# Kernel optimization log

Measured on AMD Instinct MI355X. Metric: run time of the kernel, lower is better.

The kernel has to match this reference:

```python
import jax, jax.numpy as jnp
import numpy as np

N = 100000   # nodes
E = 1250000  # directed edges
F = 32       # node_features
H = 64       # hidden_channels
C = 10       # num_classes
NEG_SLOPE = 0.2  # GATConv default LeakyReLU slope


def _glorot(key, shape):
    fan_in = shape[0]
    return jax.random.normal(key, shape, jnp.float32) / np.sqrt(fan_in)


def setup_inputs() -> dict:
    k = jax.random.split(jax.random.key(0), 16)
    x = jax.random.normal(k[0], (N, F), jnp.float32)
    edge_index = jax.random.randint(k[1], (2, E), 0, N, dtype=jnp.int32)
    return {
        "x": x,
        "edge_index": edge_index,
        # GCNConv 1
        "W1": _glorot(k[2], (F, H)), "b1": jnp.zeros((H,), jnp.float32),
        # GATConv (heads=1)
        "W2": _glorot(k[3], (H, H)),
        "a_src": _glorot(k[4], (H,)), "a_dst": _glorot(k[5], (H,)),
        "b2": jnp.zeros((H,), jnp.float32),
        # GCNConv 3
        "W3": _glorot(k[6], (H, H)), "b3": jnp.zeros((H,), jnp.float32),
        # optimization head
        "Wopt": _glorot(k[7], (H, C)), "bopt": jnp.zeros((C,), jnp.float32),
        # bottleneck detector MLP
        "Wb1": _glorot(k[8], (H, 32)), "bb1": jnp.zeros((32,), jnp.float32),
        "Wb2": _glorot(k[9], (32, 1)), "bb2": jnp.zeros((1,), jnp.float32),
    }


def _gcn_conv(x, W, b, src, dst, n):
    # PyG GCNConv: self-loops already appended to src/dst by caller.
    h = x @ W  # [n, out]
    deg = jnp.zeros((n,), x.dtype).at[dst].add(1.0)
    dinv = jax.lax.rsqrt(jnp.maximum(deg, 1e-12))
    norm = dinv[src] * dinv[dst]  # [e]
    msg = h[src] * norm[:, None]  # gather + scale
    out = jnp.zeros_like(h).at[dst].add(msg)  # scatter-add
    return out + b


def _gat_conv(x, W, a_src, a_dst, b, src, dst, n):
    # PyG GATConv, heads=1: self-loops already appended.
    h = x @ W  # [n, out]
    alpha_s = h @ a_src  # [n]
    alpha_d = h @ a_dst  # [n]
    e = jax.nn.leaky_relu(alpha_s[src] + alpha_d[dst], NEG_SLOPE)  # [e]
    # softmax over incoming edges of each dst node
    emax = jax.ops.segment_max(e, dst, num_segments=n)
    p = jnp.exp(e - emax[dst])
    denom = jax.ops.segment_sum(p, dst, num_segments=n)
    alpha = p / denom[dst]
    out = jnp.zeros_like(h).at[dst].add(h[src] * alpha[:, None])
    return out + b


def reference(x, edge_index, W1, b1, W2, a_src, a_dst, b2, W3, b3,
              Wopt, bopt, Wb1, bb1, Wb2, bb2):
    n = x.shape[0]
    loops = jnp.arange(n, dtype=edge_index.dtype)
    src = jnp.concatenate([edge_index[0], loops])
    dst = jnp.concatenate([edge_index[1], loops])

    h = jax.nn.relu(_gcn_conv(x, W1, b1, src, dst, n))
    h = jax.nn.relu(_gat_conv(h, W2, a_src, a_dst, b2, src, dst, n))
    h = jax.nn.relu(_gcn_conv(h, W3, b3, src, dst, n))

    optimizations = h @ Wopt + bopt                     # [n, C]
    bottlenecks = jax.nn.sigmoid(jax.nn.relu(h @ Wb1 + bb1) @ Wb2 + bb2)  # [n, 1]
    graph_embedding = h.mean(axis=0)                    # [H]
    return optimizations, bottlenecks, graph_embedding
```

## Files before the change

### kernel.cpp

```cpp
#include <hip/hip_runtime.h>
#include <hip/hip_bf16.h>


#define CAP 64
#define NP2 128
#define NB2MAX 800

__device__ __forceinline__ int uwave(){
  return __builtin_amdgcn_readfirstlane(threadIdx.x >> 6);
}
__device__ __forceinline__ unsigned short f2bf(float f){
  unsigned u = __float_as_uint(f);
  return (unsigned short)((u + 0x7fffu + ((u >> 16) & 1u)) >> 16);
}
__device__ __forceinline__ float bfl(unsigned u){ return __uint_as_float(u << 16); }
__device__ __forceinline__ float bfh(unsigned u){ return __uint_as_float(u & 0xffff0000u); }
__device__ __forceinline__ float bfu(unsigned short s){ return __uint_as_float(((unsigned)s) << 16); }
__device__ __forceinline__ float rdlane(float v, int l){
  return __uint_as_float(__builtin_amdgcn_readlane(__float_as_uint(v), l));
}

__global__ void k_setup(const float* __restrict__ Wopt, const float* __restrict__ bopt,
                        const float* __restrict__ Wb1, const float* __restrict__ bb1,
                        float* __restrict__ Wcat, float* __restrict__ bcat,
                        int* __restrict__ bcnt, unsigned short* __restrict__ tb,
                        unsigned short* __restrict__ xh, float* __restrict__ emb_acc,
                        int n, int nb2){
  int i = blockIdx.x*blockDim.x + threadIdx.x;
  if (i < nb2) bcnt[i] = 0;
  if (blockIdx.x == 0){
    int tid = threadIdx.x;
    for (int j = tid; j < 4096; j += 256){
      int f = j >> 6, c = j & 63;
      float w = 0.f;
      if (c < 10)       w = Wopt[f*10 + c];
      else if (c >= 32) w = Wb1[f*32 + (c-32)];
      Wcat[j] = w;
    }
    if (tid < 64){
      float b = 0.f;
      if (tid < 10)       b = bopt[tid];
      else if (tid >= 32) b = bb1[tid-32];
      bcat[tid] = b;
      tb[(size_t)n*64 + tid] = 0;
      emb_acc[tid] = 0.f;
    }
    if (tid >= 64 && tid < 96) xh[(size_t)n*32 + (tid-64)] = 0;
  }
}

__global__ __launch_bounds__(256) void k_part(const int* __restrict__ src,
                        const int* __restrict__ dst,
                        uint2* __restrict__ pairs, int* __restrict__ bcnt,
                        int e, int nb2, int pbcap){
  __shared__ int lcnt[NB2MAX];
  __shared__ int lbase[NB2MAX];
  int tid = threadIdx.x;
  for (int j = tid; j < nb2; j += 256) lcnt[j] = 0;
  __syncthreads();
  int i0 = blockIdx.x*2048 + tid*8;
  int d[8], s[8], bk[8], lp[8];
  int nv = e - i0;
  if (nv > 8) nv = 8;
  if (nv < 0) nv = 0;
  if (nv == 8){
    int4 d0 = *(const int4*)(dst + i0), d1 = *(const int4*)(dst + i0 + 4);
    int4 s0 = *(const int4*)(src + i0), s1 = *(const int4*)(src + i0 + 4);
    d[0]=d0.x; d[1]=d0.y; d[2]=d0.z; d[3]=d0.w;
    d[4]=d1.x; d[5]=d1.y; d[6]=d1.z; d[7]=d1.w;
    s[0]=s0.x; s[1]=s0.y; s[2]=s0.z; s[3]=s0.w;
    s[4]=s1.x; s[5]=s1.y; s[6]=s1.z; s[7]=s1.w;
  } else {
    #pragma unroll
    for (int j = 0; j < 8; j++){ d[j] = 0; s[j] = 0; }
    for (int j = 0; j < nv; j++){ d[j] = dst[i0+j]; s[j] = src[i0+j]; }
  }
  #pragma unroll
  for (int j = 0; j < 8; j++){
    if (j < nv){
      bk[j] = d[j] >> 7;
      lp[j] = atomicAdd(&lcnt[bk[j]], 1);
    }
  }
  __syncthreads();
  for (int j = tid; j < nb2; j += 256){
    int c = lcnt[j];
    if (c) lbase[j] = atomicAdd(&bcnt[j], c);
  }
  __syncthreads();
  #pragma unroll
  for (int j = 0; j < 8; j++){
    if (j < nv){
      int p = lbase[bk[j]] + lp[j];
      if (p < pbcap)
        pairs[(size_t)bk[j]*pbcap + p] = make_uint2((unsigned)d[j], (unsigned)s[j]);
    }
  }
}

__global__ __launch_bounds__(256) void k_fill(const uint2* __restrict__ pairs,
                        const int* __restrict__ bcnt, int* __restrict__ cnt,
                        int* __restrict__ adj, int pbcap, int n){
  __shared__ int lc[NP2];
  __shared__ int ladj[NP2*CAP];
  int b = blockIdx.x;
  int lo = b << 7;
  int nn = min(NP2, n - lo);
  int tid = threadIdx.x;
  for (int j = tid; j < NP2; j += 256) lc[j] = 0;
  __syncthreads();
  int m = bcnt[b];
  if (m > pbcap) m = pbcap;
  const uint2* pb = pairs + (size_t)b*pbcap;
  for (int j = tid; j < m; j += 256){
    uint2 p = pb[j];
    int r = (int)p.x - lo;
    int pos = atomicAdd(&lc[r], 1);
    if (pos < CAP) ladj[(r << 6) + pos] = (int)p.y;
  }
  __syncthreads();
  if (tid < nn) cnt[lo + tid] = lc[tid];
  int tot = nn << 4;
  uint4* ga = (uint4*)(adj + (size_t)lo*CAP);
  const uint4* la = (const uint4*)ladj;
  for (int j = tid; j < tot; j += 256) ga[j] = la[j];
}

__global__ void k_castscale(const float* __restrict__ x, const int* __restrict__ cnt,
                            unsigned short* __restrict__ xh, int total4){
  int i = blockIdx.x*blockDim.x + threadIdx.x;
  if (i >= total4) return;
  int row = i >> 3;
  float dv = rsqrtf((float)(cnt[row] + 1));
  float4 v = ((const float4*)x)[i];
  uint2 o;
  o.x = (unsigned)f2bf(v.x*dv) | ((unsigned)f2bf(v.y*dv) << 16);
  o.y = (unsigned)f2bf(v.z*dv) | ((unsigned)f2bf(v.w*dv) << 16);
  ((uint2*)xh)[i] = o;
}

__global__ __launch_bounds__(256) void k_agg32g(const unsigned short* __restrict__ xh,
                          const int* __restrict__ adj, const int* __restrict__ cnt,
                          const float* __restrict__ W1, const float* __restrict__ b1,
                          unsigned short* __restrict__ h, int n){
  int lane = threadIdx.x & 63;
  float wreg[32];
  #pragma unroll
  for (int k = 0; k < 32; k++) wreg[k] = W1[k*64 + lane];
  float br = b1[lane];
  int v0 = blockIdx.x*8 + uwave()*2;
  if (v0 >= n) return;
  int v1 = v0 + 1;
  bool has1 = v1 < n;
  if (!has1) v1 = v0;
  int cn0 = cnt[v0], cn1 = cnt[v1];
  int c0 = min(cn0, CAP), c1 = min(cn1, CAP);
  int ureg0 = n, ureg1 = n;
  if (lane < c0) ureg0 = (adj + (size_t)v0*CAP)[lane];
  if (lane < c1) ureg1 = (adj + (size_t)v1*CAP)[lane];
  int g = lane >> 3, q = lane & 7;
  float4 a0 = {0.f,0.f,0.f,0.f}, a1 = {0.f,0.f,0.f,0.f};
  int itm = (max(c0, c1) + 7) >> 3;
  #pragma unroll 2
  for (int jj = 0; jj < itm; jj++){
    int u0 = __shfl(ureg0, jj*8 + g);
    int u1 = __shfl(ureg1, jj*8 + g);
    uint2 r0 = ((const uint2*)(xh + (size_t)u0*32))[q];
    uint2 r1 = ((const uint2*)(xh + (size_t)u1*32))[q];
    a0.x += bfl(r0.x); a0.y += bfh(r0.x); a0.z += bfl(r0.y); a0.w += bfh(r0.y);
    a1.x += bfl(r1.x); a1.y += bfh(r1.x); a1.z += bfl(r1.y); a1.w += bfh(r1.y);
  }
  #pragma unroll
  for (int off = 8; off <= 32; off <<= 1){
    a0.x += __shfl_xor(a0.x, off); a0.y += __shfl_xor(a0.y, off);
    a0.z += __shfl_xor(a0.z, off); a0.w += __shfl_xor(a0.w, off);
    a1.x += __shfl_xor(a1.x, off); a1.y += __shfl_xor(a1.y, off);
    a1.z += __shfl_xor(a1.z, off); a1.w += __shfl_xor(a1.w, off);
  }
  uint2 s0 = ((const uint2*)(xh + (size_t)v0*32))[q];
  uint2 s1 = ((const uint2*)(xh + (size_t)v1*32))[q];
  a0.x += bfl(s0.x); a0.y += bfh(s0.x); a0.z += bfl(s0.y); a0.w += bfh(s0.y);
  a1.x += bfl(s1.x); a1.y += bfh(s1.x); a1.z += bfl(s1.y); a1.w += bfh(s1.y);
  float dv0 = rsqrtf((float)(cn0 + 1)), dv1 = rsqrtf((float)(cn1 + 1));
  a0.x *= dv0; a0.y *= dv0; a0.z *= dv0; a0.w *= dv0;
  a1.x *= dv1; a1.y *= dv1; a1.z *= dv1; a1.w *= dv1;
  float h0 = br, h1v = br;
  #pragma unroll
  for (int q2 = 0; q2 < 8; q2++){
    float w0x = rdlane(a0.x, q2), w1x = rdlane(a1.x, q2);
    float w0y = rdlane(a0.y, q2), w1y = rdlane(a1.y, q2);
    float w0z = rdlane(a0.z, q2), w1z = rdlane(a1.z, q2);
    float w0w = rdlane(a0.w, q2), w1w = rdlane(a1.w, q2);
    h0 = fmaf(w0x, wreg[q2*4+0], h0); h1v = fmaf(w1x, wreg[q2*4+0], h1v);
    h0 = fmaf(w0y, wreg[q2*4+1], h0); h1v = fmaf(w1y, wreg[q2*4+1], h1v);
    h0 = fmaf(w0z, wreg[q2*4+2], h0); h1v = fmaf(w1z, wreg[q2*4+2], h1v);
    h0 = fmaf(w0w, wreg[q2*4+3], h0); h1v = fmaf(w1w, wreg[q2*4+3], h1v);
  }
  h[(size_t)v0*64 + lane] = f2bf(fmaxf(h0, 0.f));
  if (has1) h[(size_t)v1*64 + lane] = f2bf(fmaxf(h1v, 0.f));
}

template<bool SCALE>
__global__ __launch_bounds__(256, 4) void k_gemm_b(const unsigned short* __restrict__ x,
                       const float* __restrict__ W, const int* __restrict__ cnt,
                       unsigned short* __restrict__ t, int n){
  int lane = threadIdx.x & 63;
  int gw = blockIdx.x*4 + uwave();
  int nw = gridDim.x*4;
  float wreg[64];
  #pragma unroll
  for (int k = 0; k < 64; k++) wreg[k] = W[k*64 + lane];
  for (int v = gw; v < n; v += nw){
    const uint4* xr = (const uint4*)(x + (size_t)v*64);
    float acc = 0.f;
    #pragma unroll
    for (int k8 = 0; k8 < 8; k8++){
      uint4 c = xr[k8];
      acc = fmaf(bfl(c.x), wreg[k8*8+0], acc);
      acc = fmaf(bfh(c.x), wreg[k8*8+1], acc);
      acc = fmaf(bfl(c.y), wreg[k8*8+2], acc);
      acc = fmaf(bfh(c.y), wreg[k8*8+3], acc);
      acc = fmaf(bfl(c.z), wreg[k8*8+4], acc);
      acc = fmaf(bfh(c.z), wreg[k8*8+5], acc);
      acc = fmaf(bfl(c.w), wreg[k8*8+6], acc);
      acc = fmaf(bfh(c.w), wreg[k8*8+7], acc);
    }
    if (SCALE) acc *= rsqrtf((float)(cnt[v] + 1));
    t[(size_t)v*64 + lane] = f2bf(acc);
  }
}

__global__ __launch_bounds__(256, 4) void k_gemm_alpha(const unsigned short* __restrict__ x,
                       const float* __restrict__ W,
                       const float* __restrict__ asrc, const float* __restrict__ adst,
                       unsigned short* __restrict__ t, float* __restrict__ als,
                       float* __restrict__ ald, int n){
  int lane = threadIdx.x & 63;
  int gw = blockIdx.x*4 + uwave();
  int nw = gridDim.x*4;
  float wreg[64];
  #pragma unroll
  for (int k = 0; k < 64; k++) wreg[k] = W[k*64 + lane];
  float asr = asrc[lane], adr = adst[lane];
  for (int v = gw; v < n; v += nw){
    const uint4* xr = (const uint4*)(x + (size_t)v*64);
    float acc = 0.f;
    #pragma unroll
    for (int k8 = 0; k8 < 8; k8++){
      uint4 c = xr[k8];
      acc = fmaf(bfl(c.x), wreg[k8*8+0], acc);
      acc = fmaf(bfh(c.x), wreg[k8*8+1], acc);
      acc = fmaf(bfl(c.y), wreg[k8*8+2], acc);
      acc = fmaf(bfh(c.y), wreg[k8*8+3], acc);
      acc = fmaf(bfl(c.z), wreg[k8*8+4], acc);
      acc = fmaf(bfh(c.z), wreg[k8*8+5], acc);
      acc = fmaf(bfl(c.w), wreg[k8*8+6], acc);
      acc = fmaf(bfh(c.w), wreg[k8*8+7], acc);
    }
    t[(size_t)v*64 + lane] = f2bf(acc);
    float s1 = acc * asr, s2 = acc * adr;
    #pragma unroll
    for (int off = 32; off; off >>= 1){
      s1 += __shfl_xor(s1, off);
      s2 += __shfl_xor(s2, off);
    }
    if (lane == 0){ als[v] = s1; ald[v] = s2; }
  }
}

__global__ __launch_bounds__(256) void k_gcn_agg(const unsigned short* __restrict__ t,
                          const int* __restrict__ adj, const int* __restrict__ cnt,
                          const float* __restrict__ b, unsigned short* __restrict__ h, int n){
  int lane = threadIdx.x & 63;
  int v = blockIdx.x*4 + uwave();
  if (v >= n) return;
  int cn = cnt[v];
  int c = min(cn, CAP);
  const int* row = adj + (size_t)v*CAP;
  float acc = bfu(t[(size_t)v*64 + lane]);
  int j = 0;
  for (; j + 3 < c; j += 4){
    int u0 = row[j], u1 = row[j+1], u2 = row[j+2], u3 = row[j+3];
    float x0 = bfu(t[(size_t)u0*64 + lane]);
    float x1 = bfu(t[(size_t)u1*64 + lane]);
    float x2 = bfu(t[(size_t)u2*64 + lane]);
    float x3 = bfu(t[(size_t)u3*64 + lane]);
    acc += x0; acc += x1; acc += x2; acc += x3;
  }
  for (; j < c; j++){
    int u0 = row[j];
    acc += bfu(t[(size_t)u0*64 + lane]);
  }
  float dv = rsqrtf((float)(cn + 1));
  float out = fmaxf(fmaf(acc, dv, b[lane]), 0.f);
  h[(size_t)v*64 + lane] = f2bf(out);
}

__global__ __launch_bounds__(256) void k_gat_agg(const unsigned short* __restrict__ t,
                          const int* __restrict__ adj, const int* __restrict__ cnt,
                          const float* __restrict__ als, const float* __restrict__ ald,
                          const float* __restrict__ b, unsigned short* __restrict__ h, int n){
  int lane = threadIdx.x & 63;
  int v = blockIdx.x*4 + uwave();
  if (v >= n) return;
  int c = min(cnt[v], CAP);
  const int* row = adj + (size_t)v*CAP;
  int ureg = v;
  if (lane < c) ureg = row[lane];
  float adv = ald[v];
  float e = als[ureg] + adv;
  e = e > 0.f ? e : 0.2f*e;
  float es = als[v] + adv; es = es > 0.f ? es : 0.2f*es;
  float em = (lane < c) ? e : -1e30f;
  #pragma unroll
  for (int off = 32; off; off >>= 1) em = fmaxf(em, __shfl_xor(em, off));
  em = fmaxf(em, es);
  float p = (lane < c) ? __expf(e - em) : 0.f;
  float sm = p;
  #pragma unroll
  for (int off = 32; off; off >>= 1) sm += __shfl_xor(sm, off);
  float ps = __expf(es - em);
  float inv = 1.f / (sm + ps);
  float acc = ps * bfu(t[(size_t)v*64 + lane]);
  int j = 0;
  for (; j + 3 < c; j += 4){
    int u0 = row[j], u1 = row[j+1], u2 = row[j+2], u3 = row[j+3];
    float a0 = als[u0], a1 = als[u1], a2 = als[u2], a3 = als[u3];
    float x0 = bfu(t[(size_t)u0*64 + lane]);
    float x1 = bfu(t[(size_t)u1*64 + lane]);
    float x2 = bfu(t[(size_t)u2*64 + lane]);
    float x3 = bfu(t[(size_t)u3*64 + lane]);
    float e0 = a0 + adv; e0 = e0 > 0.f ? e0 : 0.2f*e0;
    float e1 = a1 + adv; e1 = e1 > 0.f ? e1 : 0.2f*e1;
    float e2 = a2 + adv; e2 = e2 > 0.f ? e2 : 0.2f*e2;
    float e3 = a3 + adv; e3 = e3 > 0.f ? e3 : 0.2f*e3;
    acc = fmaf(__expf(e0 - em), x0, acc);
    acc = fmaf(__expf(e1 - em), x1, acc);
    acc = fmaf(__expf(e2 - em), x2, acc);
    acc = fmaf(__expf(e3 - em), x3, acc);
  }
  for (; j < c; j++){
    int u0 = row[j];
    float a0 = als[u0];
    float x0 = bfu(t[(size_t)u0*64 + lane]);
    float e0 = a0 + adv; e0 = e0 > 0.f ? e0 : 0.2f*e0;
    acc = fmaf(__expf(e0 - em), x0, acc);
  }
  float out = fmaxf(fmaf(acc, inv, b[lane]), 0.f);
  h[(size_t)v*64 + lane] = f2bf(out);
}

__global__ __launch_bounds__(256, 4) void k_heads(const unsigned short* __restrict__ h,
                        const float* __restrict__ Wcat, const float* __restrict__ bcat,
                        const float* __restrict__ Wb2, const float* __restrict__ bb2,
                        float* __restrict__ out_opt, float* __restrict__ out_bot, int n){
  int lane = threadIdx.x & 63;
  int gw = blockIdx.x*4 + uwave();
  int nw = gridDim.x*4;
  float wreg[64];
  #pragma unroll
  for (int k = 0; k < 64; k++) wreg[k] = Wcat[k*64 + lane];
  float bcr  = bcat[lane];
  float wb2r = (lane >= 32) ? Wb2[lane-32] : 0.f;
  float bb2r = bb2[0];
  for (int v = gw; v < n; v += nw){
    const uint4* xr = (const uint4*)(h + (size_t)v*64);
    float acc = bcr;
    #pragma unroll
    for (int k8 = 0; k8 < 8; k8++){
      uint4 c = xr[k8];
      acc = fmaf(bfl(c.x), wreg[k8*8+0], acc);
      acc = fmaf(bfh(c.x), wreg[k8*8+1], acc);
      acc = fmaf(bfl(c.y), wreg[k8*8+2], acc);
      acc = fmaf(bfh(c.y), wreg[k8*8+3], acc);
      acc = fmaf(bfl(c.z), wreg[k8*8+4], acc);
      acc = fmaf(bfh(c.z), wreg[k8*8+5], acc);
      acc = fmaf(bfl(c.w), wreg[k8*8+6], acc);
      acc = fmaf(bfh(c.w), wreg[k8*8+7], acc);
    }
    if (lane < 10) out_opt[(size_t)v*10 + lane] = acc;
    float contrib = fmaxf(acc, 0.f) * wb2r;
    #pragma unroll
    for (int off = 32; off; off >>= 1) contrib += __shfl_xor(contrib, off);
    if (lane == 0) out_bot[v] = 1.f / (1.f + __expf(-(contrib + bb2r)));
  }
}

__global__ __launch_bounds__(256) void k_mean(const unsigned short* __restrict__ h,
                       float* __restrict__ emb_acc, int n){
  __shared__ float red[256];
  int tid = threadIdx.x;
  int w = tid >> 6, lane = tid & 63;
  float s = 0.f;
  for (int r = blockIdx.x*4 + w; r < n; r += 1024)
    s += __uint_as_float(((unsigned)h[(size_t)r*64 + lane]) << 16);
  red[tid] = s;
  __syncthreads();
  if (tid < 64)
    atomicAdd(&emb_acc[tid], red[tid] + red[64+tid] + red[128+tid] + red[192+tid]);
}

__global__ void k_embed(const float* __restrict__ emb_acc, float* __restrict__ out_emb,
                        float invn){
  if (threadIdx.x < 64) out_emb[threadIdx.x] = emb_acc[threadIdx.x] * invn;
}

extern "C" void kernel_launch(void* const* d_in, const int* in_sizes, int n_in,
                              void* d_out, int out_size, void* d_ws, size_t ws_size,
                              hipStream_t stream) {
  const float* x    = (const float*)d_in[0];
  const int*   ei   = (const int*)d_in[1];
  const float* W1   = (const float*)d_in[2];
  const float* b1   = (const float*)d_in[3];
  const float* W2   = (const float*)d_in[4];
  const float* a_s  = (const float*)d_in[5];
  const float* a_d  = (const float*)d_in[6];
  const float* b2   = (const float*)d_in[7];
  const float* W3   = (const float*)d_in[8];
  const float* b3   = (const float*)d_in[9];
  const float* Wopt = (const float*)d_in[10];
  const float* bopt = (const float*)d_in[11];
  const float* Wb1  = (const float*)d_in[12];
  const float* bb1  = (const float*)d_in[13];
  const float* Wb2  = (const float*)d_in[14];
  const float* bb2  = (const float*)d_in[15];

  int n = in_sizes[0] / 32;
  int e = in_sizes[1] / 2;
  const int* src = ei;
  const int* dst = ei + e;

  char* ws = (char*)d_ws;
  size_t off = 0;
  auto alloc = [&](size_t bytes) -> void* {
    void* p = ws + off;
    off += (bytes + 255) & ~(size_t)255;
    return p;
  };
  int nb2 = (n + NP2 - 1) >> 7;
  int*            cnt     = (int*)           alloc((size_t)n * 4);
  int*            adj     = (int*)           alloc((size_t)n * CAP * 4);
  float*          als     = (float*)         alloc((size_t)n * 4);
  float*          ald     = (float*)         alloc((size_t)n * 4);
  unsigned short* xh      = (unsigned short*)alloc((size_t)(n+1) * 32 * 2);
  unsigned short* tb      = (unsigned short*)alloc((size_t)(n+1) * 64 * 2);
  unsigned short* hbuf    = (unsigned short*)alloc((size_t)n * 64 * 2);
  float*          emb_acc = (float*)         alloc((size_t)64 * 4);
  float*          Wcat    = (float*)         alloc((size_t)4096 * 4);
  float*          bcat    = (float*)         alloc((size_t)64 * 4);
  int*            bcnt    = (int*)           alloc((size_t)nb2 * 4);

  int pbcap = e / nb2 + 384;
  long pcap_max = ((long)n * 128) / ((long)nb2 * 8);
  if (pbcap > (int)pcap_max) pbcap = (int)pcap_max;
  uint2* pairs = (uint2*)hbuf;

  float* out_opt = (float*)d_out;
  float* out_bot = out_opt + (size_t)n * 10;
  float* out_emb = out_bot + n;

  int nb8    = (n + 7) / 8;
  int nb4    = (n + 3) / 4;
  int nbN    = (n + 255) / 256;
  int nbP    = (e + 2047) / 2048;
  int total4 = n*32/4;
  int nbC    = (total4 + 255) / 256;

  k_setup<<<nbN, 256, 0, stream>>>(Wopt, bopt, Wb1, bb1, Wcat, bcat,
                                   bcnt, tb, xh, emb_acc, n, nb2);
  k_part<<<nbP, 256, 0, stream>>>(src, dst, pairs, bcnt, e, nb2, pbcap);
  k_fill<<<nb2, 256, 0, stream>>>(pairs, bcnt, cnt, adj, pbcap, n);
  k_castscale<<<nbC, 256, 0, stream>>>(x, cnt, xh, total4);

  k_agg32g<<<nb8, 256, 0, stream>>>(xh, adj, cnt, W1, b1, hbuf, n);

  k_gemm_alpha<<<1024, 256, 0, stream>>>(hbuf, W2, a_s, a_d, tb, als, ald, n);
  k_gat_agg<<<nb4, 256, 0, stream>>>(tb, adj, cnt, als, ald, b2, hbuf, n);

  k_gemm_b<true><<<1024, 256, 0, stream>>>(hbuf, W3, cnt, tb, n);
  k_gcn_agg<<<nb4, 256, 0, stream>>>(tb, adj, cnt, b3, hbuf, n);

  k_heads<<<1024, 256, 0, stream>>>(hbuf, Wcat, bcat, Wb2, bb2,
                                    out_opt, out_bot, n);
  k_mean<<<256, 256, 0, stream>>>(hbuf, emb_acc, n);
  k_embed<<<1, 64, 0, stream>>>(emb_acc, out_emb, 1.0f / (float)n);
}
```

Before: 375.1 us.

## Process eight nodes per wavefront in GCN/GAT aggregation with 16-byte row gathers

The GCN and GAT aggregation kernels now assign 8 destination nodes per wavefront, with 8 lanes per node each loading a uint4 (8 bf16 features), instead of one node per wavefront with one feature per lane. Neighbor indices are loaded once per 8-slot block and broadcast with shuffles. The adjacency rows are pre-filled with a sentinel index n pointing at zeroed padding rows (tb and als), so lanes can run to the group-max degree without bounds checks. This is meant to cut the number of memory instructions and the per-edge index loads, at the cost of divergence padding up to the max degree among the 8 grouped nodes.

```diff
diff --git a/kernel.cpp b/kernel.cpp
--- a/kernel.cpp
+++ b/kernel.cpp
@@ -25,7 +25,7 @@
                         float* __restrict__ Wcat, float* __restrict__ bcat,
                         int* __restrict__ bcnt, unsigned short* __restrict__ tb,
                         unsigned short* __restrict__ xh, float* __restrict__ emb_acc,
-                        int n, int nb2){
+                        float* __restrict__ als, int n, int nb2){
   int i = blockIdx.x*blockDim.x + threadIdx.x;
   if (i < nb2) bcnt[i] = 0;
   if (blockIdx.x == 0){
@@ -44,6 +44,7 @@
       bcat[tid] = b;
       tb[(size_t)n*64 + tid] = 0;
       emb_acc[tid] = 0.f;
+      if (tid == 0) als[n] = 0.f;
     }
     if (tid >= 64 && tid < 96) xh[(size_t)n*32 + (tid-64)] = 0;
   }
@@ -108,6 +109,8 @@
   int nn = min(NP2, n - lo);
   int tid = threadIdx.x;
   for (int j = tid; j < NP2; j += 256) lc[j] = 0;
+  int4 nfill = make_int4(n, n, n, n);
+  for (int j = tid; j < NP2*CAP/4; j += 256) ((int4*)ladj)[j] = nfill;
   __syncthreads();
   int m = bcnt[b];
   if (m > pbcap) m = pbcap;
@@ -272,28 +275,48 @@
                           const int* __restrict__ adj, const int* __restrict__ cnt,
                           const float* __restrict__ b, unsigned short* __restrict__ h, int n){
   int lane = threadIdx.x & 63;
-  int v = blockIdx.x*4 + uwave();
-  if (v >= n) return;
-  int cn = cnt[v];
-  int c = min(cn, CAP);
-  const int* row = adj + (size_t)v*CAP;
-  float acc = bfu(t[(size_t)v*64 + lane]);
-  int j = 0;
-  for (; j + 3 < c; j += 4){
-    int u0 = row[j], u1 = row[j+1], u2 = row[j+2], u3 = row[j+3];
-    float x0 = bfu(t[(size_t)u0*64 + lane]);
-    float x1 = bfu(t[(size_t)u1*64 + lane]);
-    float x2 = bfu(t[(size_t)u2*64 + lane]);
-    float x3 = bfu(t[(size_t)u3*64 + lane]);
-    acc += x0; acc += x1; acc += x2; acc += x3;
-  }
-  for (; j < c; j++){
-    int u0 = row[j];
-    acc += bfu(t[(size_t)u0*64 + lane]);
-  }
+  int g = lane >> 3, q = lane & 7;
+  int v0 = blockIdx.x*32 + uwave()*8;
+  if (v0 >= n) return;
+  int vg = v0 + g;
+  bool vok = vg < n;
+  int vgc = vok ? vg : n - 1;
+  int cn = cnt[vgc];
+  int c = vok ? min(cn, CAP) : 0;
+  int cm = c;
+  cm = max(cm, __shfl_xor(cm, 8));
+  cm = max(cm, __shfl_xor(cm, 16));
+  cm = max(cm, __shfl_xor(cm, 32));
+  int cmax = __builtin_amdgcn_readfirstlane(cm);
+  const int* arow = adj + (size_t)vgc*CAP;
+  float a[8] = {0,0,0,0,0,0,0,0};
+  int bsel = (lane & 56);
+  for (int blk = 0; blk*8 < cmax; blk++){
+    int ureg = arow[blk*8 + q];
+    #pragma unroll
+    for (int j2 = 0; j2 < 8; j2++){
+      if (blk*8 + j2 >= cmax) break;
+      int u = __shfl(ureg, bsel | j2);
+      uint4 r = ((const uint4*)(t + (size_t)u*64))[q];
+      a[0] += bfl(r.x); a[1] += bfh(r.x); a[2] += bfl(r.y); a[3] += bfh(r.y);
+      a[4] += bfl(r.z); a[5] += bfh(r.z); a[6] += bfl(r.w); a[7] += bfh(r.w);
+    }
+  }
+  uint4 s = ((const uint4*)(t + (size_t)vgc*64))[q];
+  a[0] += bfl(s.x); a[1] += bfh(s.x); a[2] += bfl(s.y); a[3] += bfh(s.y);
+  a[4] += bfl(s.z); a[5] += bfh(s.z); a[6] += bfl(s.w); a[7] += bfh(s.w);
   float dv = rsqrtf((float)(cn + 1));
-  float out = fmaxf(fmaf(acc, dv, b[lane]), 0.f);
-  h[(size_t)v*64 + lane] = f2bf(out);
+  float4 b0 = ((const float4*)b)[2*q], b1v = ((const float4*)b)[2*q+1];
+  float r0 = fmaxf(fmaf(a[0], dv, b0.x), 0.f),  r1 = fmaxf(fmaf(a[1], dv, b0.y), 0.f);
+  float r2 = fmaxf(fmaf(a[2], dv, b0.z), 0.f),  r3 = fmaxf(fmaf(a[3], dv, b0.w), 0.f);
+  float r4 = fmaxf(fmaf(a[4], dv, b1v.x), 0.f), r5 = fmaxf(fmaf(a[5], dv, b1v.y), 0.f);
+  float r6 = fmaxf(fmaf(a[6], dv, b1v.z), 0.f), r7 = fmaxf(fmaf(a[7], dv, b1v.w), 0.f);
+  uint4 o;
+  o.x = (unsigned)f2bf(r0) | ((unsigned)f2bf(r1) << 16);
+  o.y = (unsigned)f2bf(r2) | ((unsigned)f2bf(r3) << 16);
+  o.z = (unsigned)f2bf(r4) | ((unsigned)f2bf(r5) << 16);
+  o.w = (unsigned)f2bf(r6) | ((unsigned)f2bf(r7) << 16);
+  if (vok) ((uint4*)(h + (size_t)vg*64))[q] = o;
 }
 
 __global__ __launch_bounds__(256) void k_gat_agg(const unsigned short* __restrict__ t,
@@ -301,53 +324,79 @@
                           const float* __restrict__ als, const float* __restrict__ ald,
                           const float* __restrict__ b, unsigned short* __restrict__ h, int n){
   int lane = threadIdx.x & 63;
-  int v = blockIdx.x*4 + uwave();
-  if (v >= n) return;
-  int c = min(cnt[v], CAP);
-  const int* row = adj + (size_t)v*CAP;
-  int ureg = v;
-  if (lane < c) ureg = row[lane];
-  float adv = ald[v];
-  float e = als[ureg] + adv;
-  e = e > 0.f ? e : 0.2f*e;
-  float es = als[v] + adv; es = es > 0.f ? es : 0.2f*es;
-  float em = (lane < c) ? e : -1e30f;
-  #pragma unroll
-  for (int off = 32; off; off >>= 1) em = fmaxf(em, __shfl_xor(em, off));
-  em = fmaxf(em, es);
-  float p = (lane < c) ? __expf(e - em) : 0.f;
-  float sm = p;
-  #pragma unroll
-  for (int off = 32; off; off >>= 1) sm += __shfl_xor(sm, off);
+  int g = lane >> 3, q = lane & 7;
+  int v0 = blockIdx.x*32 + uwave()*8;
+  if (v0 >= n) return;
+  int vg = v0 + g;
+  bool vok = vg < n;
+  int vgc = vok ? vg : n - 1;
+  int c = vok ? min(cnt[vgc], CAP) : 0;
+  int cm = c;
+  cm = max(cm, __shfl_xor(cm, 8));
+  cm = max(cm, __shfl_xor(cm, 16));
+  cm = max(cm, __shfl_xor(cm, 32));
+  int cmax = __builtin_amdgcn_readfirstlane(cm);
+  const int* arow = adj + (size_t)vgc*CAP;
+  float adv = ald[vgc];
+  float es = als[vgc] + adv; es = es > 0.f ? es : 0.2f*es;
+  float er[8];
+  float em = es;
+  #pragma unroll
+  for (int r = 0; r < 8; r++){
+    if (r*8 >= cmax) break;
+    int slot = r*8 + q;
+    int u = arow[slot];
+    float ev = als[u] + adv; ev = ev > 0.f ? ev : 0.2f*ev;
+    er[r] = (slot < c) ? ev : -1e30f;
+    em = fmaxf(em, er[r]);
+  }
+  em = fmaxf(em, __shfl_xor(em, 1));
+  em = fmaxf(em, __shfl_xor(em, 2));
+  em = fmaxf(em, __shfl_xor(em, 4));
+  float sm = 0.f;
+  #pragma unroll
+  for (int r = 0; r < 8; r++){
+    if (r*8 >= cmax) break;
+    sm += ((r*8 + q) < c) ? __expf(er[r] - em) : 0.f;
+  }
+  sm += __shfl_xor(sm, 1);
+  sm += __shfl_xor(sm, 2);
+  sm += __shfl_xor(sm, 4);
   float ps = __expf(es - em);
   float inv = 1.f / (sm + ps);
-  float acc = ps * bfu(t[(size_t)v*64 + lane]);
-  int j = 0;
-  for (; j + 3 < c; j += 4){
-    int u0 = row[j], u1 = row[j+1], u2 = row[j+2], u3 = row[j+3];
-    float a0 = als[u0], a1 = als[u1], a2 = als[u2], a3 = als[u3];
-    float x0 = bfu(t[(size_t)u0*64 + lane]);
-    float x1 = bfu(t[(size_t)u1*64 + lane]);
-    float x2 = bfu(t[(size_t)u2*64 + lane]);
-    float x3 = bfu(t[(size_t)u3*64 + lane]);
-    float e0 = a0 + adv; e0 = e0 > 0.f ? e0 : 0.2f*e0;
-    float e1 = a1 + adv; e1 = e1 > 0.f ? e1 : 0.2f*e1;
-    float e2 = a2 + adv; e2 = e2 > 0.f ? e2 : 0.2f*e2;
-    float e3 = a3 + adv; e3 = e3 > 0.f ? e3 : 0.2f*e3;
-    acc = fmaf(__expf(e0 - em), x0, acc);
-    acc = fmaf(__expf(e1 - em), x1, acc);
-    acc = fmaf(__expf(e2 - em), x2, acc);
-    acc = fmaf(__expf(e3 - em), x3, acc);
-  }
-  for (; j < c; j++){
-    int u0 = row[j];
-    float a0 = als[u0];
-    float x0 = bfu(t[(size_t)u0*64 + lane]);
-    float e0 = a0 + adv; e0 = e0 > 0.f ? e0 : 0.2f*e0;
-    acc = fmaf(__expf(e0 - em), x0, acc);
-  }
-  float out = fmaxf(fmaf(acc, inv, b[lane]), 0.f);
-  h[(size_t)v*64 + lane] = f2bf(out);
+  float a[8] = {0,0,0,0,0,0,0,0};
+  int bsel = (lane & 56);
+  for (int blk = 0; blk*8 < cmax; blk++){
+    int ureg = arow[blk*8 + q];
+    #pragma unroll
+    for (int j2 = 0; j2 < 8; j2++){
+      if (blk*8 + j2 >= cmax) break;
+      int u = __shfl(ureg, bsel | j2);
+      float ev = als[u] + adv; ev = ev > 0.f ? ev : 0.2f*ev;
+      float w = __expf(ev - em);
+      uint4 r = ((const uint4*)(t + (size_t)u*64))[q];
+      a[0] = fmaf(w, bfl(r.x), a[0]); a[1] = fmaf(w, bfh(r.x), a[1]);
+      a[2] = fmaf(w, bfl(r.y), a[2]); a[3] = fmaf(w, bfh(r.y), a[3]);
+      a[4] = fmaf(w, bfl(r.z), a[4]); a[5] = fmaf(w, bfh(r.z), a[5]);
+      a[6] = fmaf(w, bfl(r.w), a[6]); a[7] = fmaf(w, bfh(r.w), a[7]);
+    }
+  }
+  uint4 s = ((const uint4*)(t + (size_t)vgc*64))[q];
+  a[0] = fmaf(ps, bfl(s.x), a[0]); a[1] = fmaf(ps, bfh(s.x), a[1]);
+  a[2] = fmaf(ps, bfl(s.y), a[2]); a[3] = fmaf(ps, bfh(s.y), a[3]);
+  a[4] = fmaf(ps, bfl(s.z), a[4]); a[5] = fmaf(ps, bfh(s.z), a[5]);
+  a[6] = fmaf(ps, bfl(s.w), a[6]); a[7] = fmaf(ps, bfh(s.w), a[7]);
+  float4 b0 = ((const float4*)b)[2*q], b1v = ((const float4*)b)[2*q+1];
+  float r0 = fmaxf(fmaf(a[0], inv, b0.x), 0.f),  r1 = fmaxf(fmaf(a[1], inv, b0.y), 0.f);
+  float r2 = fmaxf(fmaf(a[2], inv, b0.z), 0.f),  r3 = fmaxf(fmaf(a[3], inv, b0.w), 0.f);
+  float r4 = fmaxf(fmaf(a[4], inv, b1v.x), 0.f), r5 = fmaxf(fmaf(a[5], inv, b1v.y), 0.f);
+  float r6 = fmaxf(fmaf(a[6], inv, b1v.z), 0.f), r7 = fmaxf(fmaf(a[7], inv, b1v.w), 0.f);
+  uint4 o;
+  o.x = (unsigned)f2bf(r0) | ((unsigned)f2bf(r1) << 16);
+  o.y = (unsigned)f2bf(r2) | ((unsigned)f2bf(r3) << 16);
+  o.z = (unsigned)f2bf(r4) | ((unsigned)f2bf(r5) << 16);
+  o.w = (unsigned)f2bf(r6) | ((unsigned)f2bf(r7) << 16);
+  if (vok) ((uint4*)(h + (size_t)vg*64))[q] = o;
 }
 
 __global__ __launch_bounds__(256, 4) void k_heads(const unsigned short* __restrict__ h,
@@ -440,7 +489,7 @@
   int nb2 = (n + NP2 - 1) >> 7;
   int*            cnt     = (int*)           alloc((size_t)n * 4);
   int*            adj     = (int*)           alloc((size_t)n * CAP * 4);
-  float*          als     = (float*)         alloc((size_t)n * 4);
+  float*          als     = (float*)         alloc((size_t)(n+1) * 4);
   float*          ald     = (float*)         alloc((size_t)n * 4);
   unsigned short* xh      = (unsigned short*)alloc((size_t)(n+1) * 32 * 2);
   unsigned short* tb      = (unsigned short*)alloc((size_t)(n+1) * 64 * 2);
@@ -460,14 +509,14 @@
   float* out_emb = out_bot + n;
 
   int nb8    = (n + 7) / 8;
-  int nb4    = (n + 3) / 4;
+  int nbW    = (n + 31) / 32;
   int nbN    = (n + 255) / 256;
   int nbP    = (e + 2047) / 2048;
   int total4 = n*32/4;
   int nbC    = (total4 + 255) / 256;
 
   k_setup<<<nbN, 256, 0, stream>>>(Wopt, bopt, Wb1, bb1, Wcat, bcat,
-                                   bcnt, tb, xh, emb_acc, n, nb2);
+                                   bcnt, tb, xh, emb_acc, als, n, nb2);
   k_part<<<nbP, 256, 0, stream>>>(src, dst, pairs, bcnt, e, nb2, pbcap);
   k_fill<<<nb2, 256, 0, stream>>>(pairs, bcnt, cnt, adj, pbcap, n);
   k_castscale<<<nbC, 256, 0, stream>>>(x, cnt, xh, total4);
@@ -475,10 +524,10 @@
   k_agg32g<<<nb8, 256, 0, stream>>>(xh, adj, cnt, W1, b1, hbuf, n);
 
   k_gemm_alpha<<<1024, 256, 0, stream>>>(hbuf, W2, a_s, a_d, tb, als, ald, n);
-  k_gat_agg<<<nb4, 256, 0, stream>>>(tb, adj, cnt, als, ald, b2, hbuf, n);
+  k_gat_agg<<<nbW, 256, 0, stream>>>(tb, adj, cnt, als, ald, b2, hbuf, n);
 
   k_gemm_b<true><<<1024, 256, 0, stream>>>(hbuf, W3, cnt, tb, n);
-  k_gcn_agg<<<nb4, 256, 0, stream>>>(tb, adj, cnt, b3, hbuf, n);
+  k_gcn_agg<<<nbW, 256, 0, stream>>>(tb, adj, cnt, b3, hbuf, n);
 
   k_heads<<<1024, 256, 0, stream>>>(hbuf, Wcat, bcat, Wb2, bb2,
                                     out_opt, out_bot, n);
```

Measured after the change: 349.3 us. 6.9% less time.
